# Performance work log

Measured on AMD Instinct MI355X. Metric: run time of the kernel, lower is better.

## Reference

```python
import jax, jax.numpy as jnp
import numpy as np

V = 6890      # SMPL vertex count
JNT = 24      # SMPL joints
NB = 10       # shape betas
PF = 207      # pose-blend features = 23*9
NJ_OUT = 19   # cocoplus joints
PARENTS = np.array([0, 0, 0, 0, 1, 2, 3, 4, 5, 6, 7, 8, 9, 9, 9, 12, 13, 14, 16, 17, 18, 19, 20, 21], dtype=np.int32)


def setup_inputs() -> dict:
    key = jax.random.key(0)
    ks = jax.random.split(key, 8)
    B = 512
    beta = jax.random.normal(ks[0], (B, NB), dtype=jnp.float32)
    theta = jax.random.normal(ks[1], (B, JNT * 3), dtype=jnp.float32)
    v_template = jax.random.normal(ks[2], (V, 3), dtype=jnp.float32)
    shapedirs = jax.random.normal(ks[3], (NB, V * 3), dtype=jnp.float32) * 0.01
    J_regressor = jax.random.uniform(ks[4], (V, JNT), dtype=jnp.float32)
    J_regressor = J_regressor / jnp.sum(J_regressor, axis=0, keepdims=True)
    posedirs = jax.random.normal(ks[5], (PF, V * 3), dtype=jnp.float32) * 0.01
    lbs_weights = jax.random.uniform(ks[6], (V, JNT), dtype=jnp.float32)
    lbs_weights = lbs_weights / jnp.sum(lbs_weights, axis=1, keepdims=True)
    joint_regressor = jax.random.uniform(ks[7], (V, NJ_OUT), dtype=jnp.float32)
    joint_regressor = joint_regressor / jnp.sum(joint_regressor, axis=0, keepdims=True)
    return {
        "beta": beta, "theta": theta, "v_template": v_template,
        "shapedirs": shapedirs, "J_regressor": J_regressor,
        "posedirs": posedirs, "lbs_weights": lbs_weights,
        "joint_regressor": joint_regressor,
    }


def batch_rodrigues(aa):
    # aa: [N,3] axis-angle -> [N,3,3] rotation via unit quaternion
    angle = jnp.linalg.norm(aa + 1e-8, axis=1, keepdims=True)  # [N,1]
    axis = aa / angle
    half = angle * 0.5
    w = jnp.cos(half)[:, 0]
    xyz = axis * jnp.sin(half)
    x, y, z = xyz[:, 0], xyz[:, 1], xyz[:, 2]
    w2, x2, y2, z2 = w * w, x * x, y * y, z * z
    wx, wy, wz = w * x, w * y, w * z
    xy, xz, yz = x * y, x * z, y * z
    R = jnp.stack([
        w2 + x2 - y2 - z2, 2 * (xy - wz), 2 * (xz + wy),
        2 * (xy + wz), w2 - x2 + y2 - z2, 2 * (yz - wx),
        2 * (xz - wy), 2 * (yz + wx), w2 - x2 - y2 + z2,
    ], axis=1).reshape(-1, 3, 3)
    return R


def _make_A(R, t):
    # R: [B,3,3], t: [B,3] -> [B,4,4]
    B = R.shape[0]
    top = jnp.concatenate([R, t[:, :, None]], axis=2)          # [B,3,4]
    bot = jnp.broadcast_to(jnp.array([0., 0., 0., 1.], R.dtype), (B, 1, 4))
    return jnp.concatenate([top, bot], axis=1)


def global_rigid_transform(Rs, J):
    # Rs: [B,24,3,3], J: [B,24,3]; kinematic-chain FK
    results = [_make_A(Rs[:, 0], J[:, 0])]
    for i in range(1, JNT):
        t = J[:, i] - J[:, PARENTS[i]]
        results.append(results[PARENTS[i]] @ _make_A(Rs[:, i], t))
    A = jnp.stack(results, axis=1)                              # [B,24,4,4]
    J_transformed = A[:, :, :3, 3]
    # remove rest-pose joint translation: A - [0 | A @ [J;0]]
    J_homo = jnp.concatenate([J, jnp.zeros_like(J[:, :, :1])], axis=2)  # [B,24,4]
    init_bone = jnp.einsum('bjpq,bjq->bjp', A, J_homo)          # [B,24,4]
    A_rel = A - jnp.concatenate(
        [jnp.zeros(A.shape[:3] + (3,), A.dtype), init_bone[..., None]], axis=-1)
    return J_transformed, A_rel


def reference(beta, theta, v_template, shapedirs, J_regressor, posedirs,
              lbs_weights, joint_regressor):
    B = beta.shape[0]
    # shape blend
    v_shaped = (beta @ shapedirs).reshape(B, V, 3) + v_template   # [B,V,3]
    # rest-pose joints
    J = jnp.einsum('bvc,vj->bjc', v_shaped, J_regressor)          # [B,24,3]
    # pose rotations
    Rs = batch_rodrigues(theta.reshape(-1, 3)).reshape(B, JNT, 3, 3)
    pose_feature = (Rs[:, 1:] - jnp.eye(3, dtype=Rs.dtype)).reshape(B, PF)
    v_posed = (pose_feature @ posedirs).reshape(B, V, 3) + v_shaped
    # FK
    _, A = global_rigid_transform(Rs, J)                          # [B,24,4,4]
    # skinning
    T = jnp.einsum('vj,bjpq->bvpq', lbs_weights, A)               # [B,V,4,4]
    v_homo = jnp.concatenate(
        [v_posed, jnp.ones((B, V, 1), v_posed.dtype)], axis=2)    # [B,V,4]
    verts = jnp.einsum('bvpq,bvq->bvp', T[:, :, :3, :], v_homo)   # [B,V,3]
    joints = jnp.einsum('bvc,vj->bjc', verts, joint_regressor)    # [B,19,3]
    return joints
```

## Files before the change

### kernel.cpp

```cpp
#include <hip/hip_runtime.h>
#include <math.h>

#define NV 6890
#define N3 20670
#define NJNT 24
#define NBETA 10
#define NPF 207
#define NJO 19
#define NBATCH 512
#define NJK 456
#define NJKP 512
#define NCOEF 218
#define PROWSP 704
#define KPAD 6912
#define KSPLIT 12
#define KCH 576
#define CSTR 224
#define CSTRV 6912

#define TRB 646
#define RODB 48
#define SJB 264
#define PMA 5913
#define PMO 27
#define PMZ 1323
#define PMT (PMA + PMO + PMZ)
#define CHB 48
#define C4R 1728
#define CMB (NJKP * C4R / 256)
#define RSP 4
#define RCH 56
#define SSTRIDE ((size_t)NBATCH * 3 * NJK)

typedef __attribute__((ext_vector_type(8))) short bfx8;
typedef __attribute__((ext_vector_type(4))) float fx4;

__constant__ int d_par[NJNT] = {0,0,0,0,1,2,3,4,5,6,7,8,9,9,9,12,13,14,16,17,18,19,20,21};
__constant__ int d_path[NJNT][9] = {
  {0,-1,-1,-1,-1,-1,-1,-1,-1},
  {0,1,-1,-1,-1,-1,-1,-1,-1},
  {0,2,-1,-1,-1,-1,-1,-1,-1},
  {0,3,-1,-1,-1,-1,-1,-1,-1},
  {0,1,4,-1,-1,-1,-1,-1,-1},
  {0,2,5,-1,-1,-1,-1,-1,-1},
  {0,3,6,-1,-1,-1,-1,-1,-1},
  {0,1,4,7,-1,-1,-1,-1,-1},
  {0,2,5,8,-1,-1,-1,-1,-1},
  {0,3,6,9,-1,-1,-1,-1,-1},
  {0,1,4,7,10,-1,-1,-1,-1},
  {0,2,5,8,11,-1,-1,-1,-1},
  {0,3,6,9,12,-1,-1,-1,-1},
  {0,3,6,9,13,-1,-1,-1,-1},
  {0,3,6,9,14,-1,-1,-1,-1},
  {0,3,6,9,12,15,-1,-1,-1},
  {0,3,6,9,13,16,-1,-1,-1},
  {0,3,6,9,14,17,-1,-1,-1},
  {0,3,6,9,13,16,18,-1,-1},
  {0,3,6,9,14,17,19,-1,-1},
  {0,3,6,9,13,16,18,20,-1},
  {0,3,6,9,14,17,19,21,-1},
  {0,3,6,9,13,16,18,20,22},
  {0,3,6,9,14,17,19,21,23}};

__device__ inline short f2bf(float f) {
  union { float f; unsigned u; } x; x.f = f;
  unsigned r = (x.u + 0x7fffu + ((x.u >> 16) & 1u)) >> 16;
  return (short)r;
}

__global__ void __launch_bounds__(256) kA(const float* __restrict__ jr,
                                          const float* __restrict__ lbs,
                                          const float* __restrict__ Jreg,
                                          const float* __restrict__ sdirs,
                                          const float* __restrict__ vtmpl,
                                          const float* __restrict__ theta,
                                          const float* __restrict__ beta,
                                          const float* __restrict__ pdirs,
                                          float* __restrict__ jrT, float* __restrict__ wT,
                                          float* __restrict__ SJ, float* __restrict__ Rs,
                                          float* __restrict__ pfc,
                                          short* __restrict__ Pb) {
  __shared__ float red[4][3];
  int bx = blockIdx.x, tid = threadIdx.x;
  if (bx < TRB) {
    int idx = bx * 256 + tid;
    if (idx < NV * NJO)  { int v = idx / NJO,  j = idx - v * NJO;  jrT[(size_t)j * CSTRV + v] = jr[idx]; }
    if (idx < NV * NJNT) {
      int v = idx / NJNT, k = idx - v * NJNT;
      wT[(size_t)k * CSTRV + v] = lbs[idx];
    }
  } else if (bx < TRB + RODB) {
    int t2 = (bx - TRB) * 256 + tid;
    int b = t2 / NJNT, j = t2 - b * NJNT;
    float a0 = theta[b * 72 + j * 3 + 0];
    float a1 = theta[b * 72 + j * 3 + 1];
    float a2 = theta[b * 72 + j * 3 + 2];
    float e0 = a0 + 1e-8f, e1 = a1 + 1e-8f, e2 = a2 + 1e-8f;
    float ang = sqrtf(e0 * e0 + e1 * e1 + e2 * e2);
    float inv = 1.0f / ang;
    float h = 0.5f * ang;
    float w = cosf(h), s = sinf(h);
    float x = a0 * inv * s, y = a1 * inv * s, z = a2 * inv * s;
    float R[9];
    R[0] = w*w + x*x - y*y - z*z; R[1] = 2.f*(x*y - w*z); R[2] = 2.f*(x*z + w*y);
    R[3] = 2.f*(x*y + w*z); R[4] = w*w - x*x + y*y - z*z; R[5] = 2.f*(y*z - w*x);
    R[6] = 2.f*(x*z - w*y); R[7] = 2.f*(y*z + w*x); R[8] = w*w - x*x - y*y + z*z;
#pragma unroll
    for (int r = 0; r < 9; ++r) Rs[b * 216 + j * 9 + r] = R[r];
    if (j >= 1) {
#pragma unroll
      for (int r = 0; r < 9; ++r)
        pfc[b * CSTR + (j - 1) * 9 + r] = R[r] - ((r % 4 == 0) ? 1.0f : 0.0f);
    } else {
#pragma unroll
      for (int i = 0; i < NBETA; ++i) pfc[b * CSTR + NPF + i] = beta[b * NBETA + i];
      pfc[b * CSTR + NPF + NBETA] = 1.0f;
    }
  } else if (bx < TRB + RODB + SJB) {
    int s = bx - TRB - RODB;
    int j = s % NJNT, k = s / NJNT;
    const float* src = (k < NBETA) ? (sdirs + (size_t)k * N3) : vtmpl;
    float a0 = 0.f, a1 = 0.f, a2 = 0.f;
    for (int v = tid; v < NV; v += 256) {
      float w = Jreg[v * NJNT + j];
      a0 += w * src[v * 3 + 0];
      a1 += w * src[v * 3 + 1];
      a2 += w * src[v * 3 + 2];
    }
    int lane = tid & 63, wid = tid >> 6;
#pragma unroll
    for (int s2 = 1; s2 < 64; s2 <<= 1) {
      a0 += __shfl_xor(a0, s2); a1 += __shfl_xor(a1, s2); a2 += __shfl_xor(a2, s2);
    }
    if (lane == 0) { red[wid][0] = a0; red[wid][1] = a1; red[wid][2] = a2; }
    __syncthreads();
    if (tid == 0) {
      float* o = SJ + (k * NJNT + j) * 3;
      o[0] = red[0][0] + red[1][0] + red[2][0] + red[3][0];
      o[1] = red[0][1] + red[1][1] + red[2][1] + red[3][1];
      o[2] = red[0][2] + red[1][2] + red[2][2] + red[3][2];
    }
  } else {
    int s4 = bx - TRB - RODB - SJB;
    if (s4 < PMA) {
      int s = s4 / 27, g = s4 - s * 27;
      const float* src; int base;
      if (s < 207)      { src = pdirs + (size_t)s * N3;         base = 3 * s; }
      else if (s < 217) { src = sdirs + (size_t)(s - 207) * N3; base = 621 + 3 * (s - 207); }
      else              { src = vtmpl;                           base = 651; }
      int v = g * 256 + tid;
      float x = 0.f, y = 0.f, z = 0.f;
      if (v < NV) { x = src[3 * v]; y = src[3 * v + 1]; z = src[3 * v + 2]; }
      Pb[(size_t)(base + 0) * KPAD + v] = f2bf(x);
      Pb[(size_t)(base + 1) * KPAD + v] = f2bf(y);
      Pb[(size_t)(base + 2) * KPAD + v] = f2bf(z);
    } else if (s4 < PMA + PMO) {
      int g = s4 - PMA;
      int v = g * 256 + tid;
      Pb[(size_t)654 * KPAD + v] = (v < NV) ? f2bf(1.0f) : (short)0;
    } else {
      int s = s4 - PMA - PMO;
      int row = 655 + s / 27, g = s % 27;
      Pb[(size_t)row * KPAD + g * 256 + tid] = (short)0;
    }
  }
}

__device__ inline void getJ(const float* __restrict__ SJ, const float* bb, int i,
                            float& o0, float& o1, float& o2) {
  int r = i * 3;
  float a0 = SJ[NBETA * 72 + r + 0];
  float a1 = SJ[NBETA * 72 + r + 1];
  float a2 = SJ[NBETA * 72 + r + 2];
#pragma unroll
  for (int k = 0; k < NBETA; ++k) {
    a0 += bb[k] * SJ[k * 72 + r + 0];
    a1 += bb[k] * SJ[k * 72 + r + 1];
    a2 += bb[k] * SJ[k * 72 + r + 2];
  }
  o0 = a0; o1 = a1; o2 = a2;
}

__global__ void __launch_bounds__(256) kB(const float* __restrict__ beta,
                                          const float* __restrict__ SJ,
                                          const float* __restrict__ Rs,
                                          const float* __restrict__ jrT,
                                          const float* __restrict__ wT,
                                          float* __restrict__ A,
                                          short* __restrict__ Cb) {
  int bx = blockIdx.x, tid = threadIdx.x;
  if (bx < CHB) {
    int idx = bx * 256 + tid;
    int b = idx / NJNT, j = idx - b * NJNT;
    const float* Rb = Rs + b * 216;
    float bb[NBETA];
#pragma unroll
    for (int k = 0; k < NBETA; ++k) bb[k] = beta[b * NBETA + k];
    float jp0, jp1, jp2;
    getJ(SJ, bb, 0, jp0, jp1, jp2);
    float T[12];
#pragma unroll
    for (int r = 0; r < 3; ++r) {
      T[r * 4 + 0] = Rb[r * 3 + 0];
      T[r * 4 + 1] = Rb[r * 3 + 1];
      T[r * 4 + 2] = Rb[r * 3 + 2];
    }
    T[3] = jp0; T[7] = jp1; T[11] = jp2;
    for (int d = 1; d < 9; ++d) {
      int i = d_path[j][d];
      if (i < 0) break;
      float ji0, ji1, ji2;
      getJ(SJ, bb, i, ji0, ji1, ji2);
      float t0 = ji0 - jp0, t1 = ji1 - jp1, t2 = ji2 - jp2;
      const float* R = Rb + i * 9;
      float R0 = R[0], R1 = R[1], R2 = R[2], R3 = R[3], R4 = R[4];
      float R5 = R[5], R6 = R[6], R7 = R[7], R8 = R[8];
#pragma unroll
      for (int r = 0; r < 3; ++r) {
        float a0 = T[r * 4 + 0], a1 = T[r * 4 + 1], a2 = T[r * 4 + 2];
        T[r * 4 + 0] = a0 * R0 + a1 * R3 + a2 * R6;
        T[r * 4 + 1] = a0 * R1 + a1 * R4 + a2 * R7;
        T[r * 4 + 2] = a0 * R2 + a1 * R5 + a2 * R8;
        T[r * 4 + 3] = a0 * t0 + a1 * t1 + a2 * t2 + T[r * 4 + 3];
      }
      jp0 = ji0; jp1 = ji1; jp2 = ji2;
    }
    float* Ab = A + b * 288 + j * 12;
#pragma unroll
    for (int r = 0; r < 3; ++r) {
      float o0 = T[r * 4 + 0], o1 = T[r * 4 + 1], o2 = T[r * 4 + 2];
      Ab[r * 4 + 0] = o0;
      Ab[r * 4 + 1] = o1;
      Ab[r * 4 + 2] = o2;
      Ab[r * 4 + 3] = T[r * 4 + 3] - (o0 * jp0 + o1 * jp1 + o2 * jp2);
    }
  } else {
    int idx = (bx - CHB) * 256 + tid;
    int jk = idx / C4R;
    int c4 = idx - jk * C4R;
    int v0 = c4 * 4;
    short4 o;
    if (jk < NJK) {
      int j = jk / NJNT, k = jk - j * NJNT;
      float4 a = *(const float4*)(jrT + (size_t)j * CSTRV + v0);
      float4 w = *(const float4*)(wT + (size_t)k * CSTRV + v0);
      o.x = (v0 + 0 < NV) ? f2bf(a.x * w.x) : (short)0;
      o.y = (v0 + 1 < NV) ? f2bf(a.y * w.y) : (short)0;
      o.z = (v0 + 2 < NV) ? f2bf(a.z * w.z) : (short)0;
      o.w = (v0 + 3 < NV) ? f2bf(a.w * w.w) : (short)0;
    } else {
      o.x = o.y = o.z = o.w = (short)0;
    }
    *(short4*)(Cb + (size_t)jk * KPAD + v0) = o;
  }
}

__global__ void __launch_bounds__(256) k_gemm(const short* __restrict__ Pb,
                                              const short* __restrict__ Cb,
                                              float* __restrict__ Dpart) {
  int m0 = blockIdx.x * 64;
  int n0 = blockIdx.y * 64;
  int kb0 = blockIdx.z * KCH;
  __shared__ __align__(16) short As[64 * 64];
  __shared__ __align__(16) short Bs[64 * 64];
  int t = threadIdx.x;
  int wid = t >> 6, lane = t & 63;
  int frow = wid * 16 + (lane & 15);
  int fgrp = lane >> 4;
  fx4 acc[4];
#pragma unroll
  for (int j = 0; j < 4; ++j)
#pragma unroll
    for (int r = 0; r < 4; ++r) acc[j][r] = 0.f;

  int c0 = t, c1 = t + 256;
  int row0 = c0 >> 3, g0 = c0 & 7, sw0 = g0 ^ (row0 & 7);
  int row1 = c1 >> 3, g1 = c1 & 7, sw1 = g1 ^ (row1 & 7);

  for (int kk = 0; kk < KCH / 64; ++kk) {
    int kb = kb0 + kk * 64;
    *(bfx8*)(As + row0 * 64 + sw0 * 8) = *(const bfx8*)(Pb + (size_t)(m0 + row0) * KPAD + kb + g0 * 8);
    *(bfx8*)(As + row1 * 64 + sw1 * 8) = *(const bfx8*)(Pb + (size_t)(m0 + row1) * KPAD + kb + g1 * 8);
    *(bfx8*)(Bs + row0 * 64 + sw0 * 8) = *(const bfx8*)(Cb + (size_t)(n0 + row0) * KPAD + kb + g0 * 8);
    *(bfx8*)(Bs + row1 * 64 + sw1 * 8) = *(const bfx8*)(Cb + (size_t)(n0 + row1) * KPAD + kb + g1 * 8);
    __syncthreads();
#pragma unroll
    for (int ks = 0; ks < 2; ++ks) {
      int ga = ks * 4 + fgrp;
      bfx8 a = *(const bfx8*)(As + frow * 64 + (ga ^ (frow & 7)) * 8);
#pragma unroll
      for (int j = 0; j < 4; ++j) {
        int bcol = j * 16 + (lane & 15);
        bfx8 b = *(const bfx8*)(Bs + bcol * 64 + (ga ^ (bcol & 7)) * 8);
        acc[j] = __builtin_amdgcn_mfma_f32_16x16x32_bf16(a, b, acc[j], 0, 0, 0);
      }
    }
    __syncthreads();
  }
  float* dst = Dpart + (size_t)blockIdx.z * PROWSP * NJKP
             + (size_t)(m0 + wid * 16 + (lane >> 4) * 4) * NJKP + n0 + (lane & 15);
#pragma unroll
  for (int j = 0; j < 4; ++j)
#pragma unroll
    for (int r = 0; r < 4; ++r)
      dst[(size_t)r * NJKP + j * 16] = acc[j][r];
}

__global__ void k_redD(const float* __restrict__ Dpart, float* __restrict__ D) {
  int i = blockIdx.x * 256 + threadIdx.x;
  if (i >= PROWSP * NJKP / 4) return;
  const float4* dp = (const float4*)Dpart;
  float4 s = dp[i];
#pragma unroll
  for (int z = 1; z < KSPLIT; ++z) {
    float4 v = dp[(size_t)z * (PROWSP * NJKP / 4) + i];
    s.x += v.x; s.y += v.y; s.z += v.z; s.w += v.w;
  }
  ((float4*)D)[i] = s;
}

__global__ void __launch_bounds__(256) k_S5b(const float* __restrict__ D,
                                             const float* __restrict__ pfc,
                                             float* __restrict__ Spart) {
  int n0 = blockIdx.x * 64;
  int b0 = blockIdx.y * 8;
  int r0 = blockIdx.z * RCH;
  int r1 = r0 + RCH; if (r1 > NCOEF) r1 = NCOEF;
  int tid = threadIdx.x;
  int jk = tid & 63;
  int bg = (tid >> 6) * 2;
  const float* Dp  = D + n0 + jk;
  const float* c0p = pfc + (size_t)(b0 + bg + 0) * CSTR;
  const float* c1p = pfc + (size_t)(b0 + bg + 1) * CSTR;
  float a00 = 0.f, a01 = 0.f, a02 = 0.f, a10 = 0.f, a11 = 0.f, a12 = 0.f;
#pragma unroll 2
  for (int r = r0; r < r1; ++r) {
    float d0 = Dp[(size_t)(3 * r + 0) * NJKP];
    float d1 = Dp[(size_t)(3 * r + 1) * NJKP];
    float d2 = Dp[(size_t)(3 * r + 2) * NJKP];
    float c0 = c0p[r];
    float c1 = c1p[r];
    a00 += c0 * d0; a01 += c0 * d1; a02 += c0 * d2;
    a10 += c1 * d0; a11 += c1 * d1; a12 += c1 * d2;
  }
  int jkg = n0 + jk;
  if (jkg < NJK) {
    float* base = Spart + (size_t)blockIdx.z * SSTRIDE;
    float* o0 = base + ((size_t)(b0 + bg + 0) * 3) * NJK + jkg;
    float* o1 = base + ((size_t)(b0 + bg + 1) * 3) * NJK + jkg;
    o0[0 * NJK] = a00; o0[1 * NJK] = a01; o0[2 * NJK] = a02;
    o1[0 * NJK] = a10; o1[1 * NJK] = a11; o1[2 * NJK] = a12;
  }
}

__global__ void k_final2(const float* __restrict__ Spart, const float* __restrict__ D,
                         const float* __restrict__ A, float* __restrict__ out) {
  int idx = blockIdx.x * 256 + threadIdx.x;
  if (idx >= NBATCH * NJO * 3) return;
  int b = idx / 57, r = idx - b * 57;
  int j = r / 3, c = r - j * 3;
  const float* c0 = D + (size_t)654 * NJKP + j * NJNT;
  const float* Sp0 = Spart + ((size_t)b * 3 + 0) * NJK + j * NJNT;
  const float* Sp1 = Spart + ((size_t)b * 3 + 1) * NJK + j * NJNT;
  const float* Sp2 = Spart + ((size_t)b * 3 + 2) * NJK + j * NJNT;
  float acc = 0.f;
#pragma unroll 4
  for (int k = 0; k < NJNT; ++k) {
    float s0 = Sp0[k], s1 = Sp1[k], s2 = Sp2[k];
#pragma unroll
    for (int z = 1; z < RSP; ++z) {
      s0 += Sp0[z * SSTRIDE + k];
      s1 += Sp1[z * SSTRIDE + k];
      s2 += Sp2[z * SSTRIDE + k];
    }
    const float* Ar = A + b * 288 + k * 12 + c * 4;
    acc += Ar[0] * s0 + Ar[1] * s1 + Ar[2] * s2 + Ar[3] * c0[k];
  }
  out[idx] = acc;
}

extern "C" void kernel_launch(void* const* d_in, const int* in_sizes, int n_in,
                              void* d_out, int out_size, void* d_ws, size_t ws_size,
                              hipStream_t stream) {
  const float* beta  = (const float*)d_in[0];
  const float* theta = (const float*)d_in[1];
  const float* vtmpl = (const float*)d_in[2];
  const float* sdirs = (const float*)d_in[3];
  const float* Jreg  = (const float*)d_in[4];
  const float* pdirs = (const float*)d_in[5];
  const float* lbs   = (const float*)d_in[6];
  const float* jreg2 = (const float*)d_in[7];
  float* out = (float*)d_out;

  float* ws    = (float*)d_ws;
  short* Cb    = (short*)ws;
  short* Pb    = Cb + (size_t)NJKP * KPAD;
  float* Dpart = (float*)(Pb + (size_t)PROWSP * KPAD);
  float* D     = Dpart + (size_t)KSPLIT * PROWSP * NJKP;
  float* Spart = D     + (size_t)PROWSP * NJKP;
  float* pfc   = Spart + (size_t)RSP * SSTRIDE;
  float* Rs    = pfc   + (size_t)NBATCH * CSTR;
  float* A     = Rs    + (size_t)NBATCH * 216;
  float* jrT   = A     + (size_t)NBATCH * 288;
  float* wT    = jrT   + (size_t)NJO * CSTRV;
  float* SJ    = wT    + (size_t)NJNT * CSTRV;

  kA<<<dim3(TRB + RODB + SJB + PMT), 256, 0, stream>>>(
      jreg2, lbs, Jreg, sdirs, vtmpl, theta, beta, pdirs,
      jrT, wT, SJ, Rs, pfc, Pb);
  kB<<<dim3(CHB + CMB), 256, 0, stream>>>(beta, SJ, Rs, jrT, wT, A, Cb);
  k_gemm<<<dim3(PROWSP / 64, NJKP / 64, KSPLIT), 256, 0, stream>>>(Pb, Cb, Dpart);
  k_redD<<<dim3(PROWSP * NJKP / 4 / 256), 256, 0, stream>>>(Dpart, D);
  k_S5b<<<dim3(NJKP / 64, NBATCH / 8, RSP), 256, 0, stream>>>(D, pfc, Spart);
  k_final2<<<dim3((NBATCH * NJO * 3 + 255) / 256), 256, 0, stream>>>(Spart, D, A, out);
}
```

Baseline: 92.93 us.

## Use LDS-tiled transpose for regressor weights and direct global-to-LDS GEMM loads

The joint regressor and skinning weight transposes in kA now stage 128 vertices at a time in shared memory, so both reads and writes are coalesced instead of scattered strided stores. The GEMM tile loads now use global_load_lds to copy bf16 data straight into LDS, skipping the register round trip. The XOR swizzle moves to the source address so the LDS layout matches the fragment reads. The direct-to-LDS path relies on per-wave contiguous destination placement and adds shared-memory use to kA.

```diff
diff --git a/kernel.cpp b/kernel.cpp
--- a/kernel.cpp
+++ b/kernel.cpp
@@ -18,7 +18,7 @@
 #define CSTR 224
 #define CSTRV 6912
 
-#define TRB 646
+#define TR2 54
 #define RODB 48
 #define SJB 264
 #define PMA 5913
@@ -34,6 +34,9 @@
 
 typedef __attribute__((ext_vector_type(8))) short bfx8;
 typedef __attribute__((ext_vector_type(4))) float fx4;
+
+#define LDSP(x) ((__attribute__((address_space(3))) void*)(x))
+#define GLBP(x) ((const __attribute__((address_space(1))) void*)(x))
 
 __constant__ int d_par[NJNT] = {0,0,0,0,1,2,3,4,5,6,7,8,9,9,9,12,13,14,16,17,18,19,20,21};
 __constant__ int d_path[NJNT][9] = {
@@ -81,16 +84,29 @@
                                           float* __restrict__ pfc,
                                           short* __restrict__ Pb) {
   __shared__ float red[4][3];
+  __shared__ float tj[128 * NJO];
+  __shared__ float tw[128 * NJNT];
   int bx = blockIdx.x, tid = threadIdx.x;
-  if (bx < TRB) {
-    int idx = bx * 256 + tid;
-    if (idx < NV * NJO)  { int v = idx / NJO,  j = idx - v * NJO;  jrT[(size_t)j * CSTRV + v] = jr[idx]; }
-    if (idx < NV * NJNT) {
-      int v = idx / NJNT, k = idx - v * NJNT;
-      wT[(size_t)k * CSTRV + v] = lbs[idx];
-    }
-  } else if (bx < TRB + RODB) {
-    int t2 = (bx - TRB) * 256 + tid;
+  if (bx < TR2) {
+    int v0 = bx * 128;
+    for (int i = tid; i < 128 * NJO; i += 256) {
+      int g = v0 * NJO + i;
+      tj[i] = (g < NV * NJO) ? jr[g] : 0.f;
+    }
+    for (int i = tid; i < 128 * NJNT; i += 256) {
+      int g = v0 * NJNT + i;
+      tw[i] = (g < NV * NJNT) ? lbs[g] : 0.f;
+    }
+    __syncthreads();
+    for (int i = tid; i < 128 * (NJO + NJNT); i += 256) {
+      int r = i >> 7, c = i & 127;
+      int v = v0 + c;
+      if (v >= NV) continue;
+      if (r < NJO) jrT[(size_t)r * CSTRV + v] = tj[c * NJO + r];
+      else         wT[(size_t)(r - NJO) * CSTRV + v] = tw[c * NJNT + (r - NJO)];
+    }
+  } else if (bx < TR2 + RODB) {
+    int t2 = (bx - TR2) * 256 + tid;
     int b = t2 / NJNT, j = t2 - b * NJNT;
     float a0 = theta[b * 72 + j * 3 + 0];
     float a1 = theta[b * 72 + j * 3 + 1];
@@ -116,8 +132,8 @@
       for (int i = 0; i < NBETA; ++i) pfc[b * CSTR + NPF + i] = beta[b * NBETA + i];
       pfc[b * CSTR + NPF + NBETA] = 1.0f;
     }
-  } else if (bx < TRB + RODB + SJB) {
-    int s = bx - TRB - RODB;
+  } else if (bx < TR2 + RODB + SJB) {
+    int s = bx - TR2 - RODB;
     int j = s % NJNT, k = s / NJNT;
     const float* src = (k < NBETA) ? (sdirs + (size_t)k * N3) : vtmpl;
     float a0 = 0.f, a1 = 0.f, a2 = 0.f;
@@ -141,7 +157,7 @@
       o[2] = red[0][2] + red[1][2] + red[2][2] + red[3][2];
     }
   } else {
-    int s4 = bx - TRB - RODB - SJB;
+    int s4 = bx - TR2 - RODB - SJB;
     if (s4 < PMA) {
       int s = s4 / 27, g = s4 - s * 27;
       const float* src; int base;
@@ -273,16 +289,25 @@
 #pragma unroll
     for (int r = 0; r < 4; ++r) acc[j][r] = 0.f;
 
-  int c0 = t, c1 = t + 256;
-  int row0 = c0 >> 3, g0 = c0 & 7, sw0 = g0 ^ (row0 & 7);
-  int row1 = c1 >> 3, g1 = c1 & 7, sw1 = g1 ^ (row1 & 7);
+  int lrow = lane >> 3;
+  int gsrc = (lane & 7) ^ lrow;
+  int rb0 = wid * 8;
+  int rb1 = 32 + wid * 8;
+  const short* srcA0 = Pb + (size_t)(m0 + rb0 + lrow) * KPAD + kb0 + gsrc * 8;
+  const short* srcA1 = Pb + (size_t)(m0 + rb1 + lrow) * KPAD + kb0 + gsrc * 8;
+  const short* srcB0 = Cb + (size_t)(n0 + rb0 + lrow) * KPAD + kb0 + gsrc * 8;
+  const short* srcB1 = Cb + (size_t)(n0 + rb1 + lrow) * KPAD + kb0 + gsrc * 8;
+  short* dstA0 = As + rb0 * 64;
+  short* dstA1 = As + rb1 * 64;
+  short* dstB0 = Bs + rb0 * 64;
+  short* dstB1 = Bs + rb1 * 64;
 
   for (int kk = 0; kk < KCH / 64; ++kk) {
-    int kb = kb0 + kk * 64;
-    *(bfx8*)(As + row0 * 64 + sw0 * 8) = *(const bfx8*)(Pb + (size_t)(m0 + row0) * KPAD + kb + g0 * 8);
-    *(bfx8*)(As + row1 * 64 + sw1 * 8) = *(const bfx8*)(Pb + (size_t)(m0 + row1) * KPAD + kb + g1 * 8);
-    *(bfx8*)(Bs + row0 * 64 + sw0 * 8) = *(const bfx8*)(Cb + (size_t)(n0 + row0) * KPAD + kb + g0 * 8);
-    *(bfx8*)(Bs + row1 * 64 + sw1 * 8) = *(const bfx8*)(Cb + (size_t)(n0 + row1) * KPAD + kb + g1 * 8);
+    __builtin_amdgcn_global_load_lds(GLBP(srcA0), LDSP(dstA0), 16, 0, 0);
+    __builtin_amdgcn_global_load_lds(GLBP(srcA1), LDSP(dstA1), 16, 0, 0);
+    __builtin_amdgcn_global_load_lds(GLBP(srcB0), LDSP(dstB0), 16, 0, 0);
+    __builtin_amdgcn_global_load_lds(GLBP(srcB1), LDSP(dstB1), 16, 0, 0);
+    srcA0 += 64; srcA1 += 64; srcB0 += 64; srcB1 += 64;
     __syncthreads();
 #pragma unroll
     for (int ks = 0; ks < 2; ++ks) {
@@ -405,7 +430,7 @@
   float* wT    = jrT   + (size_t)NJO * CSTRV;
   float* SJ    = wT    + (size_t)NJNT * CSTRV;
 
-  kA<<<dim3(TRB + RODB + SJB + PMT), 256, 0, stream>>>(
+  kA<<<dim3(TR2 + RODB + SJB + PMT), 256, 0, stream>>>(
       jreg2, lbs, Jreg, sdirs, vtmpl, theta, beta, pdirs,
       jrT, wT, SJ, Rs, pfc, Pb);
   kB<<<dim3(CHB + CMB), 256, 0, stream>>>(beta, SJ, Rs, jrT, wT, A, Cb);
```

Result: no change. 92.22 us (-0.8%).
